# Kernel optimization log

Hardware: AMD Instinct MI355X
Metric: run time of the kernel (lower is better)

The kernel has to match this reference:

```python
import jax, jax.numpy as jnp
import numpy as np

N = 262144          # nodes
E = N * 16          # edges (avg degree 16)
C_IN = 64
C_OUT = 64
GRID = 0.5          # voxel size
POS_EXTENT = 10.0   # pos in [0, 10)^3
NVOX_DIM = int(round(POS_EXTENT / GRID))  # 20
NVOX = NVOX_DIM ** 3                      # 8000 voxels
BN_EPS = 1e-5


def setup_inputs() -> dict:
    key = jax.random.key(0)
    k = jax.random.split(key, 5)
    x = jax.random.normal(k[0], (N, C_IN), dtype=jnp.float32)
    pos = jax.random.uniform(k[1], (N, 3), dtype=jnp.float32, minval=0.0, maxval=POS_EXTENT)
    edge_index = jax.random.randint(k[2], (2, E), 0, N, dtype=jnp.int32)
    W = jax.random.normal(k[3], (C_IN, C_OUT), dtype=jnp.float32) / np.float32(np.sqrt(C_IN))
    b = jnp.zeros((C_OUT,), jnp.float32)
    gamma = jnp.ones((C_OUT,), jnp.float32)
    beta = jnp.zeros((C_OUT,), jnp.float32)
    return {"x": x, "pos": pos, "edge_index": edge_index,
            "W": W, "b": b, "gamma": gamma, "beta": beta}


def reference(x, pos, edge_index, W, b, gamma, beta):
    # --- self.down: Linear -> BatchNorm1d (training-mode batch stats) -> ReLU ---
    h = x @ W + b                                   # [N, C_OUT]
    mean = jnp.mean(h, axis=0)
    var = jnp.mean(jnp.square(h - mean), axis=0)    # biased variance (torch BN)
    h = (h - mean) * jax.lax.rsqrt(var + BN_EPS) * gamma + beta
    h = jax.nn.relu(h)

    # --- max_pool_neighbor_x: scatter-max of neighbor features (self-loops added) ---
    row, col = edge_index[0], edge_index[1]
    pooled = jax.ops.segment_max(h[row], col, num_segments=N)  # [N, C_OUT]
    h = jnp.maximum(pooled, h)  # self-loop; also fixes -inf for isolated nodes

    # --- GridSampling: voxel-grid quantize + per-voxel mean of x and pos ---
    vid = jnp.clip(jnp.floor(pos / GRID).astype(jnp.int32), 0, NVOX_DIM - 1)  # [N,3]
    vox = (vid[:, 0] * NVOX_DIM + vid[:, 1]) * NVOX_DIM + vid[:, 2]           # [N]
    cnt = jax.ops.segment_sum(jnp.ones((N,), jnp.float32), vox, num_segments=NVOX)
    x_sum = jax.ops.segment_sum(h, vox, num_segments=NVOX)     # [NVOX, C_OUT]
    p_sum = jax.ops.segment_sum(pos, vox, num_segments=NVOX)   # [NVOX, 3]
    denom = jnp.maximum(cnt, 1.0)[:, None]
    x_out = x_sum / denom
    pos_out = p_sum / denom
    # concat features and positions of the downsampled graph: [NVOX, C_OUT+3]
    return jnp.concatenate([x_out, pos_out], axis=1)
```

## Files before the change

### kernel.cpp

```cpp
#include <hip/hip_runtime.h>
#include <hip/hip_fp16.h>

#define NVOX_DIM 20
#define NVOX 8000
#define BN_EPS 1e-5f

#define NBUCK 1024
#define BSHIFT 8
#define NODES_PER_BUCK 256
#define GEMM_BLOCKS 1024
#define XTRA_BLOCKS 64
#define CAP_NEW 8192
#define CAP_OLD 5120
#define VCAP 88
#define CSTRIDE 16
#define VSTRIDE 4
#define BIN_EPB 16384

typedef _Float16 f16x8 __attribute__((ext_vector_type(8)));
typedef float f32x4 __attribute__((ext_vector_type(4)));

__device__ __forceinline__ unsigned short f2key(float v) {
    unsigned short hb = __half_as_ushort(__float2half(v));
    unsigned short m = (unsigned short)(0x8000u | (unsigned short)(-(int)(hb >> 15)));
    return (unsigned short)(hb ^ m);
}

__device__ __forceinline__ float key2f(unsigned int k) {
    unsigned short hb = (k & 0x8000u) ? (unsigned short)(k ^ 0x8000u)
                                      : (unsigned short)(0xFFFFu ^ k);
    __half_raw hr;
    hr.x = hb;
    return __half2float((__half)hr);
}

__device__ __forceinline__ f16x8 pack8(float4 a, float4 b) {
    f16x8 r;
    r[0] = (_Float16)a.x; r[1] = (_Float16)a.y; r[2] = (_Float16)a.z; r[3] = (_Float16)a.w;
    r[4] = (_Float16)b.x; r[5] = (_Float16)b.y; r[6] = (_Float16)b.z; r[7] = (_Float16)b.w;
    return r;
}

__device__ __forceinline__ void gemm_step(int row0, f16x8 a0, f16x8 a1,
                                          const f16x8 (&bf)[4][2], const float (&bv)[4],
                                          float (&s)[4], float (&s2)[4],
                                          unsigned short* __restrict__ h16,
                                          int l15, int q) {
#pragma unroll
    for (int t4 = 0; t4 < 4; ++t4) {
        f32x4 acc = {bv[t4], bv[t4], bv[t4], bv[t4]};
        acc = __builtin_amdgcn_mfma_f32_16x16x32_f16(a0, bf[t4][0], acc, 0, 0, 0);
        acc = __builtin_amdgcn_mfma_f32_16x16x32_f16(a1, bf[t4][1], acc, 0, 0, 0);
        s[t4] += acc[0] + acc[1] + acc[2] + acc[3];
        s2[t4] = fmaf(acc[0], acc[0], s2[t4]);
        s2[t4] = fmaf(acc[1], acc[1], s2[t4]);
        s2[t4] = fmaf(acc[2], acc[2], s2[t4]);
        s2[t4] = fmaf(acc[3], acc[3], s2[t4]);
#pragma unroll
        for (int r = 0; r < 4; ++r) {
            h16[(size_t)(row0 + q * 4 + r) * 64 + t4 * 16 + l15] = f2key(acc[r]);
        }
    }
}

__global__ __launch_bounds__(256) void k_zero(int* __restrict__ p, int n) {
    int i = blockIdx.x * 256 + threadIdx.x;
    if (i < n) p[i] = 0;
}

__global__ __launch_bounds__(512) void k0_gemm(const float* __restrict__ x,
                                               const float* __restrict__ W,
                                               const float* __restrict__ bias,
                                               unsigned short* __restrict__ h16,
                                               float* __restrict__ partials, int n16,
                                               const float* __restrict__ pos,
                                               int* __restrict__ vcursor,
                                               int* __restrict__ vlist) {
    __shared__ float sW[4096];
    __shared__ float red[2][8][64];
    __shared__ unsigned short stg[8][16][65];
    int t = threadIdx.x;
    int bid = blockIdx.x;

    if (bid >= GEMM_BLOCKS) {
        int zb = bid - GEMM_BLOCKS;
        int nNodes = n16 * 16;
        for (int nd = zb * 512 + t; nd < nNodes; nd += XTRA_BLOCKS * 512) {
            float px = pos[(size_t)nd * 3 + 0];
            float py = pos[(size_t)nd * 3 + 1];
            float pz = pos[(size_t)nd * 3 + 2];
            int v0 = min(max((int)floorf(px * 2.f), 0), NVOX_DIM - 1);
            int v1 = min(max((int)floorf(py * 2.f), 0), NVOX_DIM - 1);
            int v2 = min(max((int)floorf(pz * 2.f), 0), NVOX_DIM - 1);
            int vox = (v0 * NVOX_DIM + v1) * NVOX_DIM + v2;
            int idx = atomicAdd(&vcursor[vox * VSTRIDE], 1);
            if (idx < VCAP) vlist[vox * VCAP + idx] = nd;
        }
        return;
    }

    int gb = bid;
    for (int i = t; i < 4096; i += 512) sW[i] = W[i];
    __syncthreads();
    int lane = t & 63;
    int w = t >> 6;
    int l15 = lane & 15;
    int q = lane >> 4;

    f16x8 bf[4][2];
#pragma unroll
    for (int t4 = 0; t4 < 4; ++t4)
#pragma unroll
        for (int kb = 0; kb < 2; ++kb)
#pragma unroll
            for (int i = 0; i < 8; ++i)
                bf[t4][kb][i] = (_Float16)sW[(kb * 32 + q * 8 + i) * 64 + t4 * 16 + l15];
    float bv[4];
#pragma unroll
    for (int t4 = 0; t4 < 4; ++t4) bv[t4] = bias[t4 * 16 + l15];

    float s[4] = {0.f, 0.f, 0.f, 0.f}, s2[4] = {0.f, 0.f, 0.f, 0.f};

    for (int g = gb * 8 + w; g < n16; g += GEMM_BLOCKS * 8) {
        int row0 = g * 16;
        const float* xp = x + (size_t)(row0 + l15) * 64 + q * 8;
        float4 xa = *(const float4*)(xp);
        float4 xb = *(const float4*)(xp + 4);
        float4 xc = *(const float4*)(xp + 32);
        float4 xd = *(const float4*)(xp + 36);
        f16x8 a0 = pack8(xa, xb), a1 = pack8(xc, xd);

#pragma unroll
        for (int t4 = 0; t4 < 4; ++t4) {
            f32x4 acc = {bv[t4], bv[t4], bv[t4], bv[t4]};
            acc = __builtin_amdgcn_mfma_f32_16x16x32_f16(a0, bf[t4][0], acc, 0, 0, 0);
            acc = __builtin_amdgcn_mfma_f32_16x16x32_f16(a1, bf[t4][1], acc, 0, 0, 0);
            s[t4] += acc[0] + acc[1] + acc[2] + acc[3];
            s2[t4] = fmaf(acc[0], acc[0], s2[t4]);
            s2[t4] = fmaf(acc[1], acc[1], s2[t4]);
            s2[t4] = fmaf(acc[2], acc[2], s2[t4]);
            s2[t4] = fmaf(acc[3], acc[3], s2[t4]);
#pragma unroll
            for (int r = 0; r < 4; ++r)
                stg[w][q * 4 + r][t4 * 16 + l15] = f2key(acc[r]);
        }
#pragma unroll
        for (int i = 0; i < 16; ++i)
            h16[(size_t)(row0 + i) * 64 + lane] = stg[w][i][lane];
    }

#pragma unroll
    for (int t4 = 0; t4 < 4; ++t4) {
        s[t4] += __shfl_xor(s[t4], 16, 64);
        s[t4] += __shfl_xor(s[t4], 32, 64);
        s2[t4] += __shfl_xor(s2[t4], 16, 64);
        s2[t4] += __shfl_xor(s2[t4], 32, 64);
    }
    if (lane < 16) {
#pragma unroll
        for (int t4 = 0; t4 < 4; ++t4) {
            red[0][w][t4 * 16 + lane] = s[t4];
            red[1][w][t4 * 16 + lane] = s2[t4];
        }
    }
    __syncthreads();
    if (t < 128) {
        int c = t & 63;
        int which = t >> 6;
        float v = 0.f;
#pragma unroll
        for (int ww = 0; ww < 8; ++ww) v += red[which][ww][c];
        partials[(size_t)gb * 128 + which * 64 + c] = v;
    }
}

__global__ __launch_bounds__(1024) void k_bin2(const int* __restrict__ rows,
                                               const int* __restrict__ cols,
                                               int* __restrict__ cursor,
                                               unsigned int* __restrict__ pairs) {
    __shared__ unsigned int buf[BIN_EPB];
    __shared__ int hist[NBUCK];
    __shared__ int wpos[NBUCK];
    __shared__ int gbase[NBUCK];
    __shared__ int wsum[16];
    int t = threadIdx.x;
    int lane = t & 63;
    int w = t >> 6;

    hist[t] = 0;
    __syncthreads();

    int base_e = blockIdx.x * BIN_EPB + t * 16;
    int r[16], c[16];
#pragma unroll
    for (int g4 = 0; g4 < 4; ++g4) {
        int e = base_e + g4 * 4;
        int4 r4 = *(const int4*)(rows + e);
        int4 c4 = *(const int4*)(cols + e);
        r[g4 * 4 + 0] = r4.x; c[g4 * 4 + 0] = c4.x;
        r[g4 * 4 + 1] = r4.y; c[g4 * 4 + 1] = c4.y;
        r[g4 * 4 + 2] = r4.z; c[g4 * 4 + 2] = c4.z;
        r[g4 * 4 + 3] = r4.w; c[g4 * 4 + 3] = c4.w;
    }
#pragma unroll
    for (int i = 0; i < 16; ++i) atomicAdd(&hist[c[i] >> BSHIFT], 1);
    __syncthreads();

    int v = hist[t];
    int inc = v;
    for (int d = 1; d < 64; d <<= 1) {
        int u = __shfl_up(inc, d, 64);
        if (lane >= d) inc += u;
    }
    if (lane == 63) wsum[w] = inc;
    __syncthreads();
    int add = 0;
    for (int ww = 0; ww < w; ++ww) add += wsum[ww];
    wpos[t] = inc - v + add;
    gbase[t] = atomicAdd(&cursor[t * CSTRIDE], v);
    __syncthreads();

#pragma unroll
    for (int i = 0; i < 16; ++i) {
        int bkt = c[i] >> BSHIFT;
        int idx = atomicAdd(&wpos[bkt], 1);
        buf[idx] = ((unsigned int)r[i] << 8) | (unsigned int)(c[i] & (NODES_PER_BUCK - 1));
    }
    __syncthreads();

    for (int it = 0; it < 64; ++it) {
        int j = w * 64 + it;
        int cnt = hist[j];
        int src = wpos[j] - cnt;
        int dst0 = gbase[j];
        for (int k2 = lane; k2 < cnt; k2 += 64) {
            int d = dst0 + k2;
            if (d < CAP_NEW) pairs[(size_t)j * CAP_NEW + d] = buf[src + k2];
        }
    }
}

__global__ __launch_bounds__(1024) void k_pool_new(const unsigned int* __restrict__ pairs_,
                                                   const int* __restrict__ cursor,
                                                   const unsigned short* __restrict__ h16,
                                                   float* __restrict__ stats2,
                                                   unsigned short* __restrict__ pooled16,
                                                   const float* __restrict__ partials,
                                                   const float* __restrict__ gamma,
                                                   const float* __restrict__ beta,
                                                   float invN) {
    __shared__ unsigned int tile[NODES_PER_BUCK * 64];
    int b = blockIdx.x;
    int t = threadIdx.x;

    if (b == NBUCK) {
        float* fred = (float*)tile;
        float* tot = ((float*)tile) + 1024;
        int c = t & 127;
        int g = t >> 7;
        float s = 0.f;
        for (int pb = g; pb < GEMM_BLOCKS; pb += 8) s += partials[(size_t)pb * 128 + c];
        fred[g * 128 + c] = s;
        __syncthreads();
        if (t < 128) {
            float v = 0.f;
#pragma unroll
            for (int g2 = 0; g2 < 8; ++g2) v += fred[g2 * 128 + t];
            tot[t] = v;
        }
        __syncthreads();
        if (t < 64) {
            float mean = tot[t] * invN;
            float var = tot[64 + t] * invN - mean * mean;
            float sc = gamma[t] * rsqrtf(var + BN_EPS);
            stats2[t] = sc;
            stats2[64 + t] = beta[t] - mean * sc;
        }
        return;
    }

    int lane = t & 63;
    int w = t >> 6;

    const unsigned int* src = (const unsigned int*)(h16 + (size_t)b * (NODES_PER_BUCK * 64));
#pragma unroll
    for (int k = 0; k < 8; ++k) {
        int i = t + k * 1024;
        unsigned int u = src[i];
        tile[2 * i] = u & 0xFFFFu;
        tile[2 * i + 1] = u >> 16;
    }
    __syncthreads();

    int cntE = min(cursor[b * CSTRIDE], CAP_NEW);
    int start = b * CAP_NEW;
    int end = start + cntE;
    int chunk = (cntE + 15) >> 4;
    int cs = start + w * chunk;
    int ce = min(cs + chunk, end);
    for (int j0 = cs; j0 < ce; j0 += 64) {
        int lim = min(64, ce - j0);
        unsigned int pk = (lane < lim) ? pairs_[j0 + lane] : 0u;
        int jj = 0;
        for (; jj + 32 <= lim; jj += 32) {
            unsigned int qv[32];
            unsigned int vv[32];
#pragma unroll
            for (int u = 0; u < 32; ++u)
                qv[u] = (unsigned int)__builtin_amdgcn_readlane((int)pk, jj + u);
#pragma unroll
            for (int u = 0; u < 32; ++u)
                vv[u] = (unsigned int)h16[(size_t)(qv[u] >> 8) * 64 + lane];
#pragma unroll
            for (int u = 0; u < 32; ++u)
                atomicMax(&tile[((qv[u] & 255u) << 6) + lane], vv[u]);
        }
        for (; jj + 8 <= lim; jj += 8) {
            unsigned int qv[8];
            unsigned int vv[8];
#pragma unroll
            for (int u = 0; u < 8; ++u)
                qv[u] = (unsigned int)__builtin_amdgcn_readlane((int)pk, jj + u);
#pragma unroll
            for (int u = 0; u < 8; ++u)
                vv[u] = (unsigned int)h16[(size_t)(qv[u] >> 8) * 64 + lane];
#pragma unroll
            for (int u = 0; u < 8; ++u)
                atomicMax(&tile[((qv[u] & 255u) << 6) + lane], vv[u]);
        }
        for (; jj < lim; ++jj) {
            unsigned int qq = (unsigned int)__builtin_amdgcn_readlane((int)pk, jj);
            unsigned int v = h16[(size_t)(qq >> 8) * 64 + lane];
            atomicMax(&tile[((qq & 255u) << 6) + lane], v);
        }
    }
    __syncthreads();

#pragma unroll
    for (int nl = 0; nl < NODES_PER_BUCK; nl += 16) {
        int node_l = nl + w;
        pooled16[((size_t)((b << BSHIFT) + node_l)) * 64 + lane] =
            (unsigned short)tile[(node_l << 6) + lane];
    }
}

__global__ __launch_bounds__(256) void k_vox(const unsigned short* __restrict__ pooled16,
                                             const int* __restrict__ vlist,
                                             const int* __restrict__ vcursor,
                                             const float* __restrict__ pos,
                                             const float* __restrict__ stats2,
                                             float* __restrict__ out) {
    int v = blockIdx.x * 4 + (threadIdx.x >> 6);
    int lane = threadIdx.x & 63;
    int cv = vcursor[v * VSTRIDE];
    int c = min(cv, VCAP);
    float scale = stats2[lane], shift = stats2[64 + lane];
    const int* lst = vlist + (size_t)v * VCAP;
    float s0 = 0.f, s1 = 0.f, s2 = 0.f, s3 = 0.f;
    int i = 0;
    for (; i + 4 <= c; i += 4) {
        int n0 = lst[i], n1 = lst[i + 1], n2 = lst[i + 2], n3 = lst[i + 3];
        float v0 = key2f(pooled16[(size_t)n0 * 64 + lane]);
        float v1 = key2f(pooled16[(size_t)n1 * 64 + lane]);
        float v2 = key2f(pooled16[(size_t)n2 * 64 + lane]);
        float v3 = key2f(pooled16[(size_t)n3 * 64 + lane]);
        s0 += fmaxf(fmaf(v0, scale, shift), 0.f);
        s1 += fmaxf(fmaf(v1, scale, shift), 0.f);
        s2 += fmaxf(fmaf(v2, scale, shift), 0.f);
        s3 += fmaxf(fmaf(v3, scale, shift), 0.f);
    }
    for (; i < c; ++i) {
        float v0 = key2f(pooled16[(size_t)lst[i] * 64 + lane]);
        s0 += fmaxf(fmaf(v0, scale, shift), 0.f);
    }
    float den = 1.f / fmaxf((float)cv, 1.f);
    out[(size_t)v * 67 + lane] = (s0 + s1 + s2 + s3) * den;
    if (lane < 3) {
        float p0 = 0.f, p1 = 0.f, p2 = 0.f, p3 = 0.f;
        int j = 0;
        for (; j + 4 <= c; j += 4) {
            p0 += pos[(size_t)lst[j] * 3 + lane];
            p1 += pos[(size_t)lst[j + 1] * 3 + lane];
            p2 += pos[(size_t)lst[j + 2] * 3 + lane];
            p3 += pos[(size_t)lst[j + 3] * 3 + lane];
        }
        for (; j < c; ++j) p0 += pos[(size_t)lst[j] * 3 + lane];
        out[(size_t)v * 67 + 64 + lane] = (p0 + p1 + p2 + p3) * den;
    }
}

__global__ __launch_bounds__(256) void k0_fused_old(const float* __restrict__ x,
                                                    const float* __restrict__ W,
                                                    const float* __restrict__ bias,
                                                    unsigned short* __restrict__ h16,
                                                    float* __restrict__ partials, int n16,
                                                    const int* __restrict__ rows,
                                                    const int* __restrict__ cols,
                                                    int* __restrict__ cursor,
                                                    unsigned int* __restrict__ pairs,
                                                    float4* __restrict__ zero_zone,
                                                    int zero_n4) {
    __shared__ float sW[4096];
    __shared__ float red[2][4][64];
    __shared__ int lh[NBUCK];
    __shared__ int lpos[NBUCK];
    int t = threadIdx.x;
    int bid = blockIdx.x;

    if (bid >= 2 * GEMM_BLOCKS) {
        int zb = bid - 2 * GEMM_BLOCKS;
        float4 z = {0.f, 0.f, 0.f, 0.f};
        for (int i = zb * 256 + t; i < zero_n4; i += XTRA_BLOCKS * 256) zero_zone[i] = z;
        return;
    }

    if (bid & 1) {
        int bb = bid >> 1;
        for (int j = t; j < NBUCK; j += 256) lh[j] = 0;
        __syncthreads();
        int base = bb * 4096 + t * 16;
        int r[16], c[16];
#pragma unroll
        for (int g4 = 0; g4 < 4; ++g4) {
            int e = base + g4 * 4;
            int4 r4 = *(const int4*)(rows + e);
            int4 c4 = *(const int4*)(cols + e);
            r[g4 * 4 + 0] = r4.x; c[g4 * 4 + 0] = c4.x;
            r[g4 * 4 + 1] = r4.y; c[g4 * 4 + 1] = c4.y;
            r[g4 * 4 + 2] = r4.z; c[g4 * 4 + 2] = c4.z;
            r[g4 * 4 + 3] = r4.w; c[g4 * 4 + 3] = c4.w;
        }
#pragma unroll
        for (int i = 0; i < 16; ++i) atomicAdd(&lh[c[i] >> BSHIFT], 1);
        __syncthreads();
        for (int j = t; j < NBUCK; j += 256) lpos[j] = atomicAdd(&cursor[j], lh[j]);
        __syncthreads();
#pragma unroll
        for (int i = 0; i < 16; ++i) {
            int bkt = c[i] >> BSHIFT;
            int idx = atomicAdd(&lpos[bkt], 1);
            if (idx < CAP_OLD)
                pairs[(size_t)bkt * CAP_OLD + idx] =
                    ((unsigned int)r[i] << 8) | (unsigned int)(c[i] & (NODES_PER_BUCK - 1));
        }
        return;
    }

    int gb = bid >> 1;
    for (int i = t; i < 4096; i += 256) sW[i] = W[i];
    __syncthreads();
    int lane = t & 63;
    int w = t >> 6;
    int l15 = lane & 15;
    int q = lane >> 4;

    f16x8 bf[4][2];
#pragma unroll
    for (int t4 = 0; t4 < 4; ++t4)
#pragma unroll
        for (int kb = 0; kb < 2; ++kb)
#pragma unroll
            for (int i = 0; i < 8; ++i)
                bf[t4][kb][i] = (_Float16)sW[(kb * 32 + q * 8 + i) * 64 + t4 * 16 + l15];
    float bv[4];
#pragma unroll
    for (int t4 = 0; t4 < 4; ++t4) bv[t4] = bias[t4 * 16 + l15];

    float s[4] = {0.f, 0.f, 0.f, 0.f}, s2[4] = {0.f, 0.f, 0.f, 0.f};

    for (int g = gb * 4 + w; g < n16; g += GEMM_BLOCKS * 4) {
        int row0 = g * 16;
        const float* xp = x + (size_t)(row0 + l15) * 64 + q * 8;
        float4 xa = *(const float4*)(xp);
        float4 xb = *(const float4*)(xp + 4);
        float4 xc = *(const float4*)(xp + 32);
        float4 xd = *(const float4*)(xp + 36);
        gemm_step(row0, pack8(xa, xb), pack8(xc, xd), bf, bv, s, s2, h16, l15, q);
    }

#pragma unroll
    for (int t4 = 0; t4 < 4; ++t4) {
        s[t4] += __shfl_xor(s[t4], 16, 64);
        s[t4] += __shfl_xor(s[t4], 32, 64);
        s2[t4] += __shfl_xor(s2[t4], 16, 64);
        s2[t4] += __shfl_xor(s2[t4], 32, 64);
    }
    if (lane < 16) {
#pragma unroll
        for (int t4 = 0; t4 < 4; ++t4) {
            red[0][w][t4 * 16 + lane] = s[t4];
            red[1][w][t4 * 16 + lane] = s2[t4];
        }
    }
    __syncthreads();
    if (t < 128) {
        int c = t & 63;
        int which = t >> 6;
        float v = red[which][0][c] + red[which][1][c] + red[which][2][c] + red[which][3][c];
        partials[(size_t)gb * 128 + which * 64 + c] = v;
    }
}

__global__ __launch_bounds__(1024) void k3_finalize(const float* __restrict__ partials,
                                                    const float* __restrict__ gamma,
                                                    const float* __restrict__ beta,
                                                    float* __restrict__ stats2, float invN) {
    __shared__ float red[8][128];
    __shared__ float tot[128];
    int t = threadIdx.x;
    int c = t & 127;
    int g = t >> 7;
    float s = 0.f;
    for (int b = g; b < GEMM_BLOCKS; b += 8) s += partials[(size_t)b * 128 + c];
    red[g][c] = s;
    __syncthreads();
    if (t < 128) {
        float v = 0.f;
#pragma unroll
        for (int g2 = 0; g2 < 8; ++g2) v += red[g2][t];
        tot[t] = v;
    }
    __syncthreads();
    if (t < 64) {
        float mean = tot[t] * invN;
        float var = tot[64 + t] * invN - mean * mean;
        float sc = gamma[t] * rsqrtf(var + BN_EPS);
        stats2[t] = sc;
        stats2[64 + t] = beta[t] - mean * sc;
    }
}

__global__ __launch_bounds__(1024) void k_pool_old(const unsigned int* __restrict__ pairs_,
                                                   const int* __restrict__ cursor,
                                                   const unsigned short* __restrict__ h16,
                                                   const float* __restrict__ pos,
                                                   const float* __restrict__ stats2,
                                                   float* __restrict__ xs,
                                                   float* __restrict__ ps,
                                                   float* __restrict__ cnt) {
    __shared__ unsigned int tile[NODES_PER_BUCK * 64];
    int b = blockIdx.x;
    int t = threadIdx.x;
    int lane = t & 63;
    int w = t >> 6;
    float scale = stats2[lane];
    float shift = stats2[64 + lane];

    const unsigned int* src = (const unsigned int*)(h16 + (size_t)b * (NODES_PER_BUCK * 64));
#pragma unroll
    for (int k = 0; k < 8; ++k) {
        int i = t + k * 1024;
        unsigned int u = src[i];
        tile[2 * i] = u & 0xFFFFu;
        tile[2 * i + 1] = u >> 16;
    }
    __syncthreads();

    int cntE = min(cursor[b], CAP_OLD);
    int start = b * CAP_OLD;
    int end = start + cntE;
    int chunk = (cntE + 15) >> 4;
    int cs = start + w * chunk;
    int ce = min(cs + chunk, end);
    for (int j0 = cs; j0 < ce; j0 += 64) {
        int lim = min(64, ce - j0);
        unsigned int pk = (lane < lim) ? pairs_[j0 + lane] : 0u;
        int jj = 0;
        for (; jj + 16 <= lim; jj += 16) {
            unsigned int qv[16];
            unsigned short vv[16];
#pragma unroll
            for (int u = 0; u < 16; ++u)
                qv[u] = (unsigned int)__builtin_amdgcn_readlane((int)pk, jj + u);
#pragma unroll
            for (int u = 0; u < 16; ++u) vv[u] = h16[(size_t)(qv[u] >> 8) * 64 + lane];
#pragma unroll
            for (int u = 0; u < 16; ++u)
                atomicMax(&tile[((qv[u] & 255u) << 6) + lane], (unsigned int)vv[u]);
        }
        for (; jj < lim; ++jj) {
            unsigned int qq = (unsigned int)__builtin_amdgcn_readlane((int)pk, jj);
            unsigned int v = h16[(size_t)(qq >> 8) * 64 + lane];
            atomicMax(&tile[((qq & 255u) << 6) + lane], v);
        }
    }
    __syncthreads();

#pragma unroll
    for (int nl = 0; nl < NODES_PER_BUCK; nl += 16) {
        int node_l = nl + w;
        int c = (b << BSHIFT) + node_l;
        float px = pos[(size_t)c * 3 + 0];
        float py = pos[(size_t)c * 3 + 1];
        float pz = pos[(size_t)c * 3 + 2];
        int v0 = min(max((int)floorf(px * 2.f), 0), NVOX_DIM - 1);
        int v1 = min(max((int)floorf(py * 2.f), 0), NVOX_DIM - 1);
        int v2 = min(max((int)floorf(pz * 2.f), 0), NVOX_DIM - 1);
        int vox = (v0 * NVOX_DIM + v1) * NVOX_DIM + v2;
        float v = key2f(tile[(node_l << 6) + lane]);
        float val = fmaxf(fmaf(v, scale, shift), 0.f);
        atomicAdd(&xs[(size_t)vox * 64 + lane], val);
        if (lane < 3) atomicAdd(&ps[vox * 3 + lane], lane == 0 ? px : (lane == 1 ? py : pz));
        if (lane == 0) atomicAdd(&cnt[vox], 1.f);
    }
}

__global__ __launch_bounds__(256) void k7_out(const float* __restrict__ xs,
                                              const float* __restrict__ ps,
                                              const float* __restrict__ cnt,
                                              float* __restrict__ out, int total) {
    int idx = blockIdx.x * blockDim.x + threadIdx.x;
    if (idx >= total) return;
    int v = idx / 67;
    int c = idx - v * 67;
    float d = fmaxf(cnt[v], 1.f);
    float val = (c < 64) ? xs[(size_t)v * 64 + c] : ps[v * 3 + (c - 64)];
    out[idx] = val / d;
}

extern "C" void kernel_launch(void* const* d_in, const int* in_sizes, int n_in,
                              void* d_out, int out_size, void* d_ws, size_t ws_size,
                              hipStream_t stream) {
    const float* x     = (const float*)d_in[0];
    const float* pos   = (const float*)d_in[1];
    const int*   ei    = (const int*)d_in[2];
    const float* W     = (const float*)d_in[3];
    const float* b     = (const float*)d_in[4];
    const float* gamma = (const float*)d_in[5];
    const float* beta  = (const float*)d_in[6];
    float* out = (float*)d_out;

    const int n = in_sizes[0] / 64;
    const int E = in_sizes[2] / 2;
    char* ws = (char*)d_ws;

    const size_t NEED_NEW = 70643712;
    if (ws_size >= NEED_NEW) {
        unsigned short* h16      = (unsigned short*)(ws + 0);
        unsigned int*   pairs    = (unsigned int*)(ws + 33554432);
        unsigned short* pooled16 = (unsigned short*)(ws + 33554432);
        float*          partials = (float*)(ws + 67108864);
        float*          stats2   = (float*)(ws + 67633152);
        int*            cursor   = (int*)(ws + 67634176);
        int*            vcursor  = (int*)(ws + 67699712);
        int*            vlist    = (int*)(ws + 67827712);

        k_zero<<<189, 256, 0, stream>>>(cursor, 48384);
        k0_gemm<<<GEMM_BLOCKS + XTRA_BLOCKS, 512, 0, stream>>>(
            x, W, b, h16, partials, n >> 4, pos, vcursor, vlist);
        k_bin2<<<E / BIN_EPB, 1024, 0, stream>>>(ei, ei + E, cursor, pairs);
        k_pool_new<<<NBUCK + 1, 1024, 0, stream>>>(pairs, cursor, h16, stats2, pooled16,
                                                   partials, gamma, beta, 1.0f / (float)n);
        k_vox<<<NVOX / 4, 256, 0, stream>>>(pooled16, vlist, vcursor, pos, stats2, out);
    } else {
        unsigned short* h16      = (unsigned short*)(ws + 0);
        unsigned int*   pairs    = (unsigned int*)(ws + 33554432);
        float*          partials = (float*)(ws + 54525952);
        float*          stats2   = (float*)(ws + 55050240);
        int*            cursor   = (int*)(ws + 55051264);
        float*          xs       = (float*)(ws + 55055360);
        float*          ps       = (float*)(ws + 57103360);
        float*          cnt      = (float*)(ws + 57199360);
        float4*         zero4    = (float4*)(ws + 55055360);
        const int zero_n4 = (57231360 - 55055360) / 16;

        k_zero<<<4, 256, 0, stream>>>(cursor, NBUCK);
        k0_fused_old<<<2 * GEMM_BLOCKS + XTRA_BLOCKS, 256, 0, stream>>>(
            x, W, b, h16, partials, n >> 4, ei, ei + E, cursor, pairs, zero4, zero_n4);
        k3_finalize<<<1, 1024, 0, stream>>>(partials, gamma, beta, stats2, 1.0f / (float)n);
        k_pool_old<<<NBUCK, 1024, 0, stream>>>(pairs, cursor, h16, pos, stats2, xs, ps, cnt);
        k7_out<<<(out_size + 255) / 256, 256, 0, stream>>>(xs, ps, cnt, out, out_size);
    }
}
```

Measured before the change: 311.5 us.

## Fuse edge binning into GEMM kernel launch with interleaved block roles

Merges the edge-binning kernel into the GEMM/voxel front kernel. Every third block bins 8192 edges with 512 threads, the other two run the GEMM, and the remaining blocks build voxel lists. Shared memory is a union sized for both roles. This removes a kernel launch and lets the bandwidth-bound binning overlap with the MFMA GEMM. In exchange, each binning block handles half as many edges, so there are twice as many global cursor atomics.

Result: no change. 310.3 us (-0.4%).

```diff
diff --git a/kernel.cpp b/kernel.cpp
--- a/kernel.cpp
+++ b/kernel.cpp
@@ -9,13 +9,14 @@
 #define BSHIFT 8
 #define NODES_PER_BUCK 256
 #define GEMM_BLOCKS 1024
+#define BIN_BLOCKS 512
 #define XTRA_BLOCKS 64
 #define CAP_NEW 8192
 #define CAP_OLD 5120
 #define VCAP 88
 #define CSTRIDE 16
 #define VSTRIDE 4
-#define BIN_EPB 16384
+#define BIN_EPB 8192
 
 typedef _Float16 f16x8 __attribute__((ext_vector_type(8)));
 typedef float f32x4 __attribute__((ext_vector_type(4)));
@@ -68,22 +69,40 @@
     if (i < n) p[i] = 0;
 }
 
-__global__ __launch_bounds__(512) void k0_gemm(const float* __restrict__ x,
+__global__ __launch_bounds__(512) void k_front(const float* __restrict__ x,
                                                const float* __restrict__ W,
                                                const float* __restrict__ bias,
                                                unsigned short* __restrict__ h16,
                                                float* __restrict__ partials, int n16,
+                                               const int* __restrict__ rows,
+                                               const int* __restrict__ cols,
+                                               int* __restrict__ cursor,
+                                               unsigned int* __restrict__ pairs,
                                                const float* __restrict__ pos,
                                                int* __restrict__ vcursor,
                                                int* __restrict__ vlist) {
-    __shared__ float sW[4096];
-    __shared__ float red[2][8][64];
-    __shared__ unsigned short stg[8][16][65];
+    union SharedU {
+        struct {
+            float sW[4096];
+            float red[2][8][64];
+            unsigned short stg[8][16][65];
+        } g;
+        struct {
+            unsigned int buf[BIN_EPB];
+            int hist[NBUCK];
+            int wpos[NBUCK];
+            int gbase[NBUCK];
+            int wsum[8];
+        } b;
+    };
+    __shared__ SharedU su;
     int t = threadIdx.x;
     int bid = blockIdx.x;
-
-    if (bid >= GEMM_BLOCKS) {
-        int zb = bid - GEMM_BLOCKS;
+    int lane = t & 63;
+    int w = t >> 6;
+
+    if (bid >= GEMM_BLOCKS + BIN_BLOCKS) {
+        int zb = bid - (GEMM_BLOCKS + BIN_BLOCKS);
         int nNodes = n16 * 16;
         for (int nd = zb * 512 + t; nd < nNodes; nd += XTRA_BLOCKS * 512) {
             float px = pos[(size_t)nd * 3 + 0];
@@ -99,11 +118,72 @@
         return;
     }
 
-    int gb = bid;
-    for (int i = t; i < 4096; i += 512) sW[i] = W[i];
-    __syncthreads();
-    int lane = t & 63;
-    int w = t >> 6;
+    if ((bid % 3) == 2) {
+        int bb = bid / 3;
+        su.b.hist[t] = 0;
+        su.b.hist[t + 512] = 0;
+        __syncthreads();
+
+        int base_e = bb * BIN_EPB + t * 16;
+        int r[16], c[16];
+#pragma unroll
+        for (int g4 = 0; g4 < 4; ++g4) {
+            int e = base_e + g4 * 4;
+            int4 r4 = *(const int4*)(rows + e);
+            int4 c4 = *(const int4*)(cols + e);
+            r[g4 * 4 + 0] = r4.x; c[g4 * 4 + 0] = c4.x;
+            r[g4 * 4 + 1] = r4.y; c[g4 * 4 + 1] = c4.y;
+            r[g4 * 4 + 2] = r4.z; c[g4 * 4 + 2] = c4.z;
+            r[g4 * 4 + 3] = r4.w; c[g4 * 4 + 3] = c4.w;
+        }
+#pragma unroll
+        for (int i = 0; i < 16; ++i) atomicAdd(&su.b.hist[c[i] >> BSHIFT], 1);
+        __syncthreads();
+
+        int c0 = su.b.hist[2 * t];
+        int c1 = su.b.hist[2 * t + 1];
+        int p = c0 + c1;
+        int inc = p;
+        for (int d = 1; d < 64; d <<= 1) {
+            int u = __shfl_up(inc, d, 64);
+            if (lane >= d) inc += u;
+        }
+        if (lane == 63) su.b.wsum[w] = inc;
+        __syncthreads();
+        int add = 0;
+        for (int ww = 0; ww < w; ++ww) add += su.b.wsum[ww];
+        int base = inc - p + add;
+        su.b.wpos[2 * t] = base;
+        su.b.wpos[2 * t + 1] = base + c0;
+        su.b.gbase[2 * t] = atomicAdd(&cursor[(2 * t) * CSTRIDE], c0);
+        su.b.gbase[2 * t + 1] = atomicAdd(&cursor[(2 * t + 1) * CSTRIDE], c1);
+        __syncthreads();
+
+#pragma unroll
+        for (int i = 0; i < 16; ++i) {
+            int bkt = c[i] >> BSHIFT;
+            int idx = atomicAdd(&su.b.wpos[bkt], 1);
+            su.b.buf[idx] = ((unsigned int)r[i] << 8) |
+                            (unsigned int)(c[i] & (NODES_PER_BUCK - 1));
+        }
+        __syncthreads();
+
+        for (int it = 0; it < 128; ++it) {
+            int j = w * 128 + it;
+            int cnt = su.b.hist[j];
+            int src = su.b.wpos[j] - cnt;
+            int dst0 = su.b.gbase[j];
+            for (int k2 = lane; k2 < cnt; k2 += 64) {
+                int d = dst0 + k2;
+                if (d < CAP_NEW) pairs[(size_t)j * CAP_NEW + d] = su.b.buf[src + k2];
+            }
+        }
+        return;
+    }
+
+    int gb = (bid / 3) * 2 + (bid % 3);
+    for (int i = t; i < 4096; i += 512) su.g.sW[i] = W[i];
+    __syncthreads();
     int l15 = lane & 15;
     int q = lane >> 4;
 
@@ -114,7 +194,7 @@
         for (int kb = 0; kb < 2; ++kb)
 #pragma unroll
             for (int i = 0; i < 8; ++i)
-                bf[t4][kb][i] = (_Float16)sW[(kb * 32 + q * 8 + i) * 64 + t4 * 16 + l15];
+                bf[t4][kb][i] = (_Float16)su.g.sW[(kb * 32 + q * 8 + i) * 64 + t4 * 16 + l15];
     float bv[4];
 #pragma unroll
     for (int t4 = 0; t4 < 4; ++t4) bv[t4] = bias[t4 * 16 + l15];
@@ -142,11 +222,11 @@
             s2[t4] = fmaf(acc[3], acc[3], s2[t4]);
 #pragma unroll
             for (int r = 0; r < 4; ++r)
-                stg[w][q * 4 + r][t4 * 16 + l15] = f2key(acc[r]);
+                su.g.stg[w][q * 4 + r][t4 * 16 + l15] = f2key(acc[r]);
         }
 #pragma unroll
         for (int i = 0; i < 16; ++i)
-            h16[(size_t)(row0 + i) * 64 + lane] = stg[w][i][lane];
+            h16[(size_t)(row0 + i) * 64 + lane] = su.g.stg[w][i][lane];
     }
 
 #pragma unroll
@@ -159,8 +239,8 @@
     if (lane < 16) {
 #pragma unroll
         for (int t4 = 0; t4 < 4; ++t4) {
-            red[0][w][t4 * 16 + lane] = s[t4];
-            red[1][w][t4 * 16 + lane] = s2[t4];
+            su.g.red[0][w][t4 * 16 + lane] = s[t4];
+            su.g.red[1][w][t4 * 16 + lane] = s2[t4];
         }
     }
     __syncthreads();
@@ -169,74 +249,8 @@
         int which = t >> 6;
         float v = 0.f;
 #pragma unroll
-        for (int ww = 0; ww < 8; ++ww) v += red[which][ww][c];
+        for (int ww = 0; ww < 8; ++ww) v += su.g.red[which][ww][c];
         partials[(size_t)gb * 128 + which * 64 + c] = v;
-    }
-}
-
-__global__ __launch_bounds__(1024) void k_bin2(const int* __restrict__ rows,
-                                               const int* __restrict__ cols,
-                                               int* __restrict__ cursor,
-                                               unsigned int* __restrict__ pairs) {
-    __shared__ unsigned int buf[BIN_EPB];
-    __shared__ int hist[NBUCK];
-    __shared__ int wpos[NBUCK];
-    __shared__ int gbase[NBUCK];
-    __shared__ int wsum[16];
-    int t = threadIdx.x;
-    int lane = t & 63;
-    int w = t >> 6;
-
-    hist[t] = 0;
-    __syncthreads();
-
-    int base_e = blockIdx.x * BIN_EPB + t * 16;
-    int r[16], c[16];
-#pragma unroll
-    for (int g4 = 0; g4 < 4; ++g4) {
-        int e = base_e + g4 * 4;
-        int4 r4 = *(const int4*)(rows + e);
-        int4 c4 = *(const int4*)(cols + e);
-        r[g4 * 4 + 0] = r4.x; c[g4 * 4 + 0] = c4.x;
-        r[g4 * 4 + 1] = r4.y; c[g4 * 4 + 1] = c4.y;
-        r[g4 * 4 + 2] = r4.z; c[g4 * 4 + 2] = c4.z;
-        r[g4 * 4 + 3] = r4.w; c[g4 * 4 + 3] = c4.w;
-    }
-#pragma unroll
-    for (int i = 0; i < 16; ++i) atomicAdd(&hist[c[i] >> BSHIFT], 1);
-    __syncthreads();
-
-    int v = hist[t];
-    int inc = v;
-    for (int d = 1; d < 64; d <<= 1) {
-        int u = __shfl_up(inc, d, 64);
-        if (lane >= d) inc += u;
-    }
-    if (lane == 63) wsum[w] = inc;
-    __syncthreads();
-    int add = 0;
-    for (int ww = 0; ww < w; ++ww) add += wsum[ww];
-    wpos[t] = inc - v + add;
-    gbase[t] = atomicAdd(&cursor[t * CSTRIDE], v);
-    __syncthreads();
-
-#pragma unroll
-    for (int i = 0; i < 16; ++i) {
-        int bkt = c[i] >> BSHIFT;
-        int idx = atomicAdd(&wpos[bkt], 1);
-        buf[idx] = ((unsigned int)r[i] << 8) | (unsigned int)(c[i] & (NODES_PER_BUCK - 1));
-    }
-    __syncthreads();
-
-    for (int it = 0; it < 64; ++it) {
-        int j = w * 64 + it;
-        int cnt = hist[j];
-        int src = wpos[j] - cnt;
-        int dst0 = gbase[j];
-        for (int k2 = lane; k2 < cnt; k2 += 64) {
-            int d = dst0 + k2;
-            if (d < CAP_NEW) pairs[(size_t)j * CAP_NEW + d] = buf[src + k2];
-        }
     }
 }
 
@@ -646,9 +660,9 @@
         int*            vlist    = (int*)(ws + 67827712);
 
         k_zero<<<189, 256, 0, stream>>>(cursor, 48384);
-        k0_gemm<<<GEMM_BLOCKS + XTRA_BLOCKS, 512, 0, stream>>>(
-            x, W, b, h16, partials, n >> 4, pos, vcursor, vlist);
-        k_bin2<<<E / BIN_EPB, 1024, 0, stream>>>(ei, ei + E, cursor, pairs);
+        k_front<<<GEMM_BLOCKS + BIN_BLOCKS + XTRA_BLOCKS, 512, 0, stream>>>(
+            x, W, b, h16, partials, n >> 4, ei, ei + E, cursor, pairs,
+            pos, vcursor, vlist);
         k_pool_new<<<NBUCK + 1, 1024, 0, stream>>>(pairs, cursor, h16, stats2, pooled16,
                                                    partials, gamma, beta, 1.0f / (float)n);
         k_vox<<<NVOX / 4, 256, 0, stream>>>(pooled16, vlist, vcursor, pos, stats2, out);
```
